# Kernel tuning notes

Measured on AMD Instinct MI355X. Metric: run time of the kernel, lower is better.

Reference implementation:

```python
import math
import jax, jax.numpy as jnp
import numpy as np

B, N, D, H = 2, 8192, 1024, 16


def setup_inputs() -> dict:
    key = jax.random.key(0)
    k1, k2, k3, k4 = jax.random.split(key, 4)
    s = 1.0 / math.sqrt(D)
    return {
        "x": jax.random.normal(k1, (B, N, D), dtype=jnp.float32),
        "W_qk": jax.random.normal(k2, (D, D), dtype=jnp.float32) * s,
        "W_v": jax.random.normal(k3, (D, D), dtype=jnp.float32) * s,
        "W_out": jax.random.normal(k4, (D, D), dtype=jnp.float32) * s,
        "tau": jnp.ones((H, 1, 1), dtype=jnp.float32),
    }


def reference(x, W_qk, W_v, W_out, tau):
    b, n, d = x.shape
    h = H
    dh = d // h
    # QK / V projections (no bias), then to channel-major (B, H, dh, N)
    qk = (x @ W_qk).transpose(0, 2, 1).reshape(b, h, dh, n)
    v = (x @ W_v).transpose(0, 2, 1).reshape(b, h, dh, n)
    # Cross-channel Gram matrix over tokens: (B, H, dh, dh)
    dot = jnp.einsum('bhcn,bhdn->bhcd', qk, qk)
    q2 = jnp.sum(qk * qk, axis=-1)  # (B, H, dh)
    # Negative squared Euclidean distance between channel vectors
    logits = (2.0 * dot - q2[:, :, :, None] - q2[:, :, None, :]) / math.sqrt(max(n, 1))
    logits = logits * tau[None, ...]
    attn = jax.nn.softmax(logits, axis=-1)  # (B, H, dh, dh)
    w = jnp.einsum('bhcd,bhdn->bhcn', attn, v)  # (B, H, dh, N)
    out = w.reshape(b, d, n).transpose(0, 2, 1) @ W_out  # (B, N, D)
    return out
```

## Files before the change

### kernel.cpp

```cpp
#include <hip/hip_runtime.h>
#include <hip/hip_bf16.h>
#include <cstdint>
#include <cstddef>

typedef __bf16 v8bf __attribute__((ext_vector_type(8)));
typedef float  v4f  __attribute__((ext_vector_type(4)));

__device__ __forceinline__ unsigned short f2bf(float f) {
    unsigned int u = __float_as_uint(f);
    u += 0x7fffu + ((u >> 16) & 1u);
    return (unsigned short)(u >> 16);
}

__device__ __forceinline__ void gload_lds16(const unsigned short* g, unsigned short* l) {
    __builtin_amdgcn_global_load_lds(
        (const __attribute__((address_space(1))) unsigned int*)(uintptr_t)g,
        (__attribute__((address_space(3))) unsigned int*)(uintptr_t)l, 16, 0, 0);
}

template<int WRITE_BF16>
__global__ __launch_bounds__(256, 2) void gemm_bt(
    const unsigned short* __restrict__ A,
    const unsigned short* __restrict__ BT,
    void* __restrict__ C,
    int K, int lda, int ldb, int ldc,
    size_t sAz, size_t sBz, size_t sCz,
    int nBlk, int mPerXcd)
{
    __shared__ unsigned short sA[128 * 32];
    __shared__ unsigned short sB[128 * 32];

    const int id = blockIdx.x;
    const int xcd = id & 7;
    int s = id >> 3;
    const int perXcd = mPerXcd * nBlk;
    const int z = s / perXcd;
    s -= z * perXcd;
    const int mB = xcd * mPerXcd + s / nBlk;
    const int nB = s - (s / nBlk) * nBlk;

    const unsigned short* Ab = A + (size_t)z * sAz;
    const unsigned short* Bb = BT + (size_t)z * sBz;

    const int tid  = threadIdx.x;
    const int wv   = tid >> 6;
    const int lane = tid & 63;
    const int quad = lane >> 4;
    const int l16  = lane & 15;
    const size_t bm = (size_t)mB * 128;
    const size_t bn = (size_t)nB * 128;
    const int wm = (wv >> 1) * 64;
    const int wn = (wv & 1) * 64;

    const int ro = tid >> 2;
    const int ko = (((tid & 3) ^ (ro & 3)) << 3);

    const unsigned short* aptr0 = Ab + (bm + ro)      * (size_t)lda + ko;
    const unsigned short* aptr1 = Ab + (bm + ro + 64) * (size_t)lda + ko;
    const unsigned short* bptr0 = Bb + (bn + ro)      * (size_t)ldb + ko;
    const unsigned short* bptr1 = Bb + (bn + ro + 64) * (size_t)ldb + ko;

    unsigned short* sA0 = &sA[wv * 512];
    unsigned short* sA1 = &sA[2048 + wv * 512];
    unsigned short* sB0 = &sB[wv * 512];
    unsigned short* sB1 = &sB[2048 + wv * 512];

    const int sslot = ((quad ^ (l16 & 3)) << 3);

    v4f acc[4][4] = {};

    for (int k0 = 0; k0 < K; k0 += 32) {
        gload_lds16(aptr0 + k0, sA0);
        gload_lds16(aptr1 + k0, sA1);
        gload_lds16(bptr0 + k0, sB0);
        gload_lds16(bptr1 + k0, sB1);
        __syncthreads();

        v8bf af[4], bfr[4];
        #pragma unroll
        for (int t = 0; t < 4; t++) {
            af[t]  = *(const v8bf*)&sA[(size_t)(wm + t * 16 + l16) * 32 + sslot];
            bfr[t] = *(const v8bf*)&sB[(size_t)(wn + t * 16 + l16) * 32 + sslot];
        }

        #pragma unroll
        for (int ti = 0; ti < 4; ti++)
            #pragma unroll
            for (int tj = 0; tj < 4; tj++)
                acc[ti][tj] = __builtin_amdgcn_mfma_f32_16x16x32_bf16(
                    af[ti], bfr[tj], acc[ti][tj], 0, 0, 0);
        __syncthreads();
    }

    if (WRITE_BF16) {
        unsigned short* Cb = (unsigned short*)C + (size_t)z * sCz;
        #pragma unroll
        for (int ti = 0; ti < 4; ti++) {
            const size_t row0 = bm + wm + ti * 16 + quad * 4;
            #pragma unroll
            for (int tj = 0; tj < 4; tj++) {
                const size_t col = bn + wn + tj * 16 + l16;
                #pragma unroll
                for (int r = 0; r < 4; r++)
                    Cb[(row0 + r) * (size_t)ldc + col] = f2bf(acc[ti][tj][r]);
            }
        }
    } else {
        float* Cb = (float*)C + (size_t)z * sCz;
        #pragma unroll
        for (int ti = 0; ti < 4; ti++) {
            const size_t row0 = bm + wm + ti * 16 + quad * 4;
            #pragma unroll
            for (int tj = 0; tj < 4; tj++) {
                const size_t col = bn + wn + tj * 16 + l16;
                #pragma unroll
                for (int r = 0; r < 4; r++)
                    Cb[(row0 + r) * (size_t)ldc + col] = acc[ti][tj][r];
            }
        }
    }
}

#define MFMA_Q(MH, NH, BF)                                                    \
    do {                                                                      \
        __builtin_amdgcn_s_setprio(1);                                        \
        _Pragma("unroll")                                                     \
        for (int mi = 0; mi < 4; ++mi) {                                      \
            _Pragma("unroll")                                                 \
            for (int ni = 0; ni < 2; ++ni) {                                  \
                acc[(MH)*4 + mi][(NH)*2 + ni] =                               \
                    __builtin_amdgcn_mfma_f32_16x16x32_bf16(                  \
                        aF[mi][0], BF[ni][0],                                 \
                        acc[(MH)*4 + mi][(NH)*2 + ni], 0, 0, 0);              \
                acc[(MH)*4 + mi][(NH)*2 + ni] =                               \
                    __builtin_amdgcn_mfma_f32_16x16x32_bf16(                  \
                        aF[mi][1], BF[ni][1],                                 \
                        acc[(MH)*4 + mi][(NH)*2 + ni], 0, 0, 0);              \
            }                                                                 \
        }                                                                     \
        __builtin_amdgcn_s_setprio(0);                                        \
    } while (0)

#define RD_A(BASE)                                                            \
    do {                                                                      \
        _Pragma("unroll")                                                     \
        for (int mi = 0; mi < 4; ++mi) {                                      \
            aF[mi][0] = *(const v8bf*)((BASE) + (arow0 + mi * 1024));         \
            aF[mi][1] = *(const v8bf*)((BASE) + ((arow0 + mi * 1024) ^ 32));  \
        }                                                                     \
    } while (0)

#define RD_B(DST, BASE)                                                       \
    do {                                                                      \
        _Pragma("unroll")                                                     \
        for (int ni = 0; ni < 2; ++ni) {                                      \
            DST[ni][0] = *(const v8bf*)((BASE) + (brow0 + ni * 1024));        \
            DST[ni][1] = *(const v8bf*)((BASE) + ((brow0 + ni * 1024) ^ 32)); \
        }                                                                     \
    } while (0)

#define GTILE(T, P, B0CUR, B0NXT)                                             \
    do {                                                                      \
        const unsigned short* sa = sm + (P) * 16384;                          \
        const unsigned short* sb = sm + 32768 + (P) * 16384;                  \
        unsigned short* dq = sm + ((P) ^ 1) * 16384;                          \
        unsigned short* dp = sm + (P) * 16384;                                \
        const int kk1 = ((T) + 1) * 64, kk2 = ((T) + 2) * 64;                 \
                                                       \
        RD_A(sa);                                                             \
        if ((T) + 1 < NT) {                                                   \
            gload_lds16(aP + 128 * lda + kk1, dq + 8192 + stA);               \
            gload_lds16(aP + 192 * lda + kk1, dq + 8192 + stA + 4096);        \
        }                                                                     \
        __builtin_amdgcn_s_barrier();                                         \
        asm volatile("s_waitcnt lgkmcnt(0)" ::: "memory");                    \
        __builtin_amdgcn_sched_barrier(0);                                    \
        MFMA_Q(0, 0, B0CUR);                                                  \
        __builtin_amdgcn_s_barrier();                                         \
                                                       \
        RD_B(b1, sb + 8192);                                                  \
        if ((T) + 2 < NT) {                                                   \
            gload_lds16(aP + kk2,            dp + stA);                       \
            gload_lds16(aP + 64 * lda + kk2, dp + stA + 4096);                \
        }                                                                     \
        __builtin_amdgcn_s_barrier();                                         \
        asm volatile("s_waitcnt lgkmcnt(0)" ::: "memory");                    \
        __builtin_amdgcn_sched_barrier(0);                                    \
        MFMA_Q(0, 1, b1);                                                     \
        __builtin_amdgcn_s_barrier();                                         \
                                                       \
        RD_A(sa + 8192);                                                      \
        if ((T) + 2 < NT) {                                                   \
            gload_lds16(bP + kk2,            dp + 32768 + stA);               \
            gload_lds16(bP + 64 * ldb + kk2, dp + 32768 + stA + 4096);        \
        }                                                                     \
        __builtin_amdgcn_s_barrier();                                         \
        asm volatile("s_waitcnt lgkmcnt(0)" ::: "memory");                    \
        __builtin_amdgcn_sched_barrier(0);                                    \
        MFMA_Q(1, 1, b1);                                                     \
        __builtin_amdgcn_s_barrier();                                         \
                                                       \
        if ((T) + 2 < NT) {                                                   \
            gload_lds16(bP + 128 * ldb + kk2, dp + 32768 + 8192 + stA);       \
            gload_lds16(bP + 192 * ldb + kk2, dp + 32768 + 8192 + stA + 4096);\
            asm volatile("s_waitcnt vmcnt(6)" ::: "memory");                  \
        } else {                                                              \
            asm volatile("s_waitcnt vmcnt(0)" ::: "memory");                  \
        }                                                                     \
        if ((T) + 1 < NT) {                                                   \
            RD_B(B0NXT, sm + 32768 + ((P) ^ 1) * 16384);                      \
            asm volatile("" ::: "memory");                                    \
        }                                                                     \
        __builtin_amdgcn_s_barrier();                                         \
        MFMA_Q(1, 0, B0CUR);                                                  \
        __builtin_amdgcn_s_barrier();                                         \
    } while (0)

template<int WRITE_BF16>
__global__ __launch_bounds__(512, 2) void gemm256_bt(
    const unsigned short* __restrict__ A,
    const unsigned short* __restrict__ BT,
    void* __restrict__ C,
    int K, int lda, int ldb, int ldc,
    size_t sAz, size_t sBz, size_t sCz,
    int nBlk, int mPerXcd)
{
    __shared__ unsigned short sm[65536];

    const int id = blockIdx.x;
    const int xcd = id & 7;
    int s = id >> 3;
    const int perXcd = mPerXcd * nBlk;
    const int z = s / perXcd;
    s -= z * perXcd;
    const int mB = xcd * mPerXcd + s / nBlk;
    const int nB = s - (s / nBlk) * nBlk;

    const unsigned short* Ab = A + (size_t)z * sAz;
    const unsigned short* Bb = BT + (size_t)z * sBz;

    const int tid  = threadIdx.x;
    const int wv   = tid >> 6;
    const int lane = tid & 63;
    const int quad = lane >> 4;
    const int l16  = lane & 15;
    const int wm   = wv >> 2;
    const int wn   = wv & 3;

    const size_t bm = (size_t)mB * 256;
    const size_t bn = (size_t)nB * 256;

    const int r0   = tid >> 3;
    const int slog = (tid & 7) ^ (r0 & 7);
    const unsigned short* aP = Ab + (bm + r0) * (size_t)lda + slog * 8;
    const unsigned short* bP = Bb + (bn + r0) * (size_t)ldb + slog * 8;

    const int stA = wv * 512;

    const int soff0 = (quad ^ (l16 & 7)) * 8;
    const int arow0 = (wm * 64 + l16) * 64 + soff0;
    const int brow0 = (wn * 32 + l16) * 64 + soff0;

    v4f  acc[8][4] = {};
    v8bf aF[4][2];
    v8bf b1[2][2];
    v8bf b0a[2][2];
    v8bf b0b[2][2];

    const int NT = K >> 6;

    {
        gload_lds16(aP,                sm + stA);
        gload_lds16(aP + 64 * lda,     sm + stA + 4096);
        gload_lds16(aP + 128 * lda,    sm + 8192 + stA);
        gload_lds16(aP + 192 * lda,    sm + 8192 + stA + 4096);
        gload_lds16(bP,                sm + 32768 + stA);
        gload_lds16(bP + 64 * ldb,     sm + 32768 + stA + 4096);
        gload_lds16(bP + 128 * ldb,    sm + 32768 + 8192 + stA);
        gload_lds16(bP + 192 * ldb,    sm + 32768 + 8192 + stA + 4096);
        gload_lds16(aP + 64,                 sm + 16384 + stA);
        gload_lds16(aP + 64 * lda + 64,      sm + 16384 + stA + 4096);
        gload_lds16(bP + 64,                 sm + 32768 + 16384 + stA);
        gload_lds16(bP + 64 * ldb + 64,      sm + 32768 + 16384 + stA + 4096);
        gload_lds16(bP + 128 * ldb + 64,     sm + 32768 + 16384 + 8192 + stA);
        gload_lds16(bP + 192 * ldb + 64,     sm + 32768 + 16384 + 8192 + stA + 4096);
        asm volatile("s_waitcnt vmcnt(6)" ::: "memory");
        __builtin_amdgcn_s_barrier();
        RD_B(b0a, sm + 32768);
        asm volatile("" ::: "memory");
    }

    for (int it = 0; it < (NT >> 1); ++it) {
        const int t0 = it * 2;
        GTILE(t0,     0, b0a, b0b);
        GTILE(t0 + 1, 1, b0b, b0a);
    }

    if (WRITE_BF16) {
        unsigned short* Cb = (unsigned short*)C + (size_t)z * sCz;
        #pragma unroll
        for (int mh = 0; mh < 2; ++mh)
            #pragma unroll
            for (int mi = 0; mi < 4; ++mi) {
                const size_t row0 = bm + mh * 128 + wm * 64 + mi * 16 + quad * 4;
                #pragma unroll
                for (int nh = 0; nh < 2; ++nh)
                    #pragma unroll
                    for (int ni = 0; ni < 2; ++ni) {
                        const size_t col = bn + nh * 128 + wn * 32 + ni * 16 + l16;
                        #pragma unroll
                        for (int r = 0; r < 4; ++r)
                            Cb[(row0 + r) * (size_t)ldc + col] =
                                f2bf(acc[mh * 4 + mi][nh * 2 + ni][r]);
                    }
            }
    } else {
        float* Cb = (float*)C + (size_t)z * sCz;
        #pragma unroll
        for (int mh = 0; mh < 2; ++mh)
            #pragma unroll
            for (int mi = 0; mi < 4; ++mi) {
                const size_t row0 = bm + mh * 128 + wm * 64 + mi * 16 + quad * 4;
                #pragma unroll
                for (int nh = 0; nh < 2; ++nh)
                    #pragma unroll
                    for (int ni = 0; ni < 2; ++ni) {
                        const size_t col = bn + nh * 128 + wn * 32 + ni * 16 + l16;
                        #pragma unroll
                        for (int r = 0; r < 4; ++r)
                            Cb[(row0 + r) * (size_t)ldc + col] =
                                acc[mh * 4 + mi][nh * 2 + ni][r];
                    }
            }
    }
}
#undef GTILE
#undef RD_A
#undef RD_B
#undef MFMA_Q

__global__ __launch_bounds__(256) void gram_kernel(
    const unsigned short* __restrict__ qk,
    float* __restrict__ partial)
{
    const int bh = blockIdx.x;
    const int split = blockIdx.y;
    const int b = bh >> 4, h = bh & 15;
    const unsigned short* base = qk + (size_t)b * 8192 * 1024 + (size_t)h * 64;
    const int n0 = split * 512;

    __shared__ unsigned short sMT[64 * 136];
    const int tid = threadIdx.x;
    const int wv = tid >> 6, lane = tid & 63, quad = lane >> 4, l16 = lane & 15;

    uint4 pre[4];
    #pragma unroll
    for (int i = 0; i < 4; i++) {
        const int ch = tid + i * 256, tok = ch >> 3, co = (ch & 7) << 3;
        pre[i] = *(const uint4*)(base + (size_t)(n0 + tok) * 1024 + co);
    }

    v4f acc[4] = {};

    for (int chunk = 0; chunk < 4; chunk++) {
        __syncthreads();
        #pragma unroll
        for (int i = 0; i < 4; i++) {
            const int ch = tid + i * 256, tok = ch >> 3, co = (ch & 7) << 3;
            union { uint4 v; unsigned short s8[8]; } u; u.v = pre[i];
            #pragma unroll
            for (int j = 0; j < 8; j++)
                sMT[(size_t)(co + j) * 136 + tok] = u.s8[j];
        }
        __syncthreads();

        if (chunk < 3) {
            const int nb = n0 + (chunk + 1) * 128;
            #pragma unroll
            for (int i = 0; i < 4; i++) {
                const int ch = tid + i * 256, tok = ch >> 3, co = (ch & 7) << 3;
                pre[i] = *(const uint4*)(base + (size_t)(nb + tok) * 1024 + co);
            }
        }

        #pragma unroll
        for (int ks = 0; ks < 4; ks++) {
            const int kb = ks * 32 + quad * 8;
            const v8bf a = *(const v8bf*)&sMT[(size_t)(16 * wv + l16) * 136 + kb];
            #pragma unroll
            for (int t = 0; t < 4; t++) {
                const v8bf bb = *(const v8bf*)&sMT[(size_t)(t * 16 + l16) * 136 + kb];
                acc[t] = __builtin_amdgcn_mfma_f32_16x16x32_bf16(a, bb, acc[t], 0, 0, 0);
            }
        }
    }

    float* outp = partial + ((size_t)split * 32 + bh) * 4096;
    #pragma unroll
    for (int t = 0; t < 4; t++)
        #pragma unroll
        for (int r = 0; r < 4; r++)
            outp[(size_t)(16 * wv + quad * 4 + r) * 64 + t * 16 + l16] = acc[t][r];
}

__global__ __launch_bounds__(256) void softmax_kernel(
    const float* __restrict__ partial,
    const float* __restrict__ tau,
    float* __restrict__ attnT)
{
    const int gw = (int)((blockIdx.x * 256 + threadIdx.x) >> 6);
    const int d = threadIdx.x & 63;
    const int bh = gw >> 6;
    const int c = gw & 63;
    const int h = bh & 15;

    float cd = 0.f, cc = 0.f, dd = 0.f;
    #pragma unroll
    for (int s = 0; s < 16; s++) {
        const float* p = partial + ((size_t)s * 32 + bh) * 4096;
        cd += p[c * 64 + d];
        cc += p[c * 65];
        dd += p[d * 65];
    }
    const float INV_SQRT_N = 0.011048543456039806f;
    const float logit = (2.f * cd - cc - dd) * INV_SQRT_N * tau[h];

    float m = logit;
    #pragma unroll
    for (int off = 32; off > 0; off >>= 1) m = fmaxf(m, __shfl_xor(m, off, 64));
    const float e = __expf(logit - m);
    float sum = e;
    #pragma unroll
    for (int off = 32; off > 0; off >>= 1) sum += __shfl_xor(sum, off, 64);

    attnT[(size_t)bh * 4096 + d * 64 + c] = e / sum;
}

__global__ __launch_bounds__(256) void wefft_kernel(
    const float* __restrict__ attnT,
    const float* __restrict__ Wout,
    unsigned short* __restrict__ weffT)
{
    const int bh = blockIdx.x;
    const int jg = blockIdx.y;
    const int b = bh >> 4, h = bh & 15;

    __shared__ float sAttT[64][65];
    __shared__ float sW[64][65];
    const int tid = threadIdx.x;
    const float* ap = attnT + (size_t)bh * 4096;
    const float* wp = Wout + (size_t)(h * 64) * 1024 + jg * 64;
    for (int i = tid; i < 4096; i += 256) {
        const int r = i >> 6, q = i & 63;
        sAttT[r][q] = ap[i];
        sW[r][q] = wp[(size_t)r * 1024 + q];
    }
    __syncthreads();

    const int dd0 = (tid >> 4) << 2;
    const int j0  = (tid & 15) << 2;
    float acc[4][4] = {};
    for (int cc = 0; cc < 64; cc++) {
        float av[4], wvv[4];
        #pragma unroll
        for (int i = 0; i < 4; i++) av[i] = sAttT[dd0 + i][cc];
        #pragma unroll
        for (int i = 0; i < 4; i++) wvv[i] = sW[cc][j0 + i];
        #pragma unroll
        for (int i = 0; i < 4; i++)
            #pragma unroll
            for (int j = 0; j < 4; j++)
                acc[i][j] += av[i] * wvv[j];
    }

    unsigned short* op = weffT + ((size_t)b * 1024 + jg * 64) * 1024 + h * 64;
    #pragma unroll
    for (int i = 0; i < 4; i++)
        #pragma unroll
        for (int j = 0; j < 4; j++)
            op[(size_t)(j0 + j) * 1024 + dd0 + i] = f2bf(acc[i][j]);
}

__global__ __launch_bounds__(256) void cvt_all_kernel(
    const float* __restrict__ x, const float* __restrict__ Wv,
    const float* __restrict__ Wqk,
    unsigned short* __restrict__ xb, unsigned short* __restrict__ wvb,
    unsigned short* __restrict__ wqkT)
{
    const int bid = blockIdx.x;
    if (bid < 17408) {
        const float* src = (bid < 16384) ? x : Wv;
        unsigned short* dst = (bid < 16384) ? xb : wvb;
        const size_t blk = (bid < 16384) ? bid : (bid - 16384);
        const size_t i = (blk * 256 + threadIdx.x) * 4;
        const float4 v = *(const float4*)(src + i);
        ushort4 o;
        o.x = f2bf(v.x); o.y = f2bf(v.y); o.z = f2bf(v.z); o.w = f2bf(v.w);
        *(ushort4*)(dst + i) = o;
    } else {
        const int t = bid - 17408;
        const int n0 = (t & 31) * 32, k0 = (t >> 5) * 32;
        __shared__ float sT[32][33];
        const int tx = threadIdx.x & 31, ty = threadIdx.x >> 5;
        #pragma unroll
        for (int i = ty; i < 32; i += 8)
            sT[i][tx] = Wqk[(size_t)(k0 + i) * 1024 + n0 + tx];
        __syncthreads();
        #pragma unroll
        for (int i = ty; i < 32; i += 8)
            wqkT[(size_t)(n0 + i) * 1024 + k0 + tx] = f2bf(sT[tx][i]);
    }
}

extern "C" void kernel_launch(void* const* d_in, const int* in_sizes, int n_in,
                              void* d_out, int out_size, void* d_ws, size_t ws_size,
                              hipStream_t stream)
{
    (void)in_sizes; (void)n_in; (void)out_size; (void)ws_size;
    const float* x    = (const float*)d_in[0];
    const float* Wqk  = (const float*)d_in[1];
    const float* Wv   = (const float*)d_in[2];
    const float* Wout = (const float*)d_in[3];
    const float* tau  = (const float*)d_in[4];

    unsigned short* xb     = (unsigned short*)d_ws;
    unsigned short* wqkT   = xb + (size_t)16384 * 1024;
    unsigned short* wvb    = wqkT + (size_t)1024 * 1024;
    unsigned short* qk     = wvb + (size_t)1024 * 1024;
    float*          partial= (float*)(qk + (size_t)16384 * 1024);
    float*          attnT  = partial + (size_t)16 * 32 * 4096;
    unsigned short* weffT  = (unsigned short*)(attnT + (size_t)32 * 4096);
    unsigned short* wfoldT = weffT + (size_t)2 * 1024 * 1024;

    cvt_all_kernel<<<18432, 256, 0, stream>>>(x, Wv, Wqk, xb, wvb, wqkT);

    gemm256_bt<1><<<256, 512, 0, stream>>>(
        xb, wqkT, (void*)qk, 1024, 1024, 1024, 1024, 0, 0, 0, 4, 8);

    gram_kernel<<<dim3(32, 16), 256, 0, stream>>>(qk, partial);
    softmax_kernel<<<512, 256, 0, stream>>>(partial, tau, attnT);
    wefft_kernel<<<dim3(32, 16), 256, 0, stream>>>(attnT, Wout, weffT);

    gemm_bt<1><<<128, 256, 0, stream>>>(
        weffT, wvb, (void*)wfoldT, 1024, 1024, 1024, 1024,
        (size_t)1024 * 1024, 0, (size_t)1024 * 1024, 8, 1);

    gemm256_bt<0><<<256, 512, 0, stream>>>(
        xb, wfoldT, d_out, 1024, 1024, 1024, 1024,
        (size_t)8192 * 1024, (size_t)1024 * 1024, (size_t)8192 * 1024, 4, 4);
}
```

Measured before the change: 264.4 us.

## Produce QK projection channel-major so gram kernel reads it without transposing

The QK projection GEMM now swaps its operands (W_qk^T times x^T), so it writes qk in channel-major layout (1024 x 16384). A new swapBig flag keeps the XCD-aware block mapping on the large dimension. The gram kernel then loads whole 64x512 channel slices straight into a swizzled LDS buffer with async global-to-LDS copies, replacing the per-element transpose through shared memory. The GEMM macro helpers are inlined and the sched_barriers removed, which leaves the compiler freer to reorder instructions but loosens the hand-tuned schedule.

```diff
diff --git a/kernel.cpp b/kernel.cpp
--- a/kernel.cpp
+++ b/kernel.cpp
@@ -141,24 +141,6 @@
         __builtin_amdgcn_s_setprio(0);                                        \
     } while (0)
 
-#define RD_A(BASE)                                                            \
-    do {                                                                      \
-        _Pragma("unroll")                                                     \
-        for (int mi = 0; mi < 4; ++mi) {                                      \
-            aF[mi][0] = *(const v8bf*)((BASE) + (arow0 + mi * 1024));         \
-            aF[mi][1] = *(const v8bf*)((BASE) + ((arow0 + mi * 1024) ^ 32));  \
-        }                                                                     \
-    } while (0)
-
-#define RD_B(DST, BASE)                                                       \
-    do {                                                                      \
-        _Pragma("unroll")                                                     \
-        for (int ni = 0; ni < 2; ++ni) {                                      \
-            DST[ni][0] = *(const v8bf*)((BASE) + (brow0 + ni * 1024));        \
-            DST[ni][1] = *(const v8bf*)((BASE) + ((brow0 + ni * 1024) ^ 32)); \
-        }                                                                     \
-    } while (0)
-
 #define GTILE(T, P, B0CUR, B0NXT)                                             \
     do {                                                                      \
         const unsigned short* sa = sm + (P) * 16384;                          \
@@ -166,40 +148,49 @@
         unsigned short* dq = sm + ((P) ^ 1) * 16384;                          \
         unsigned short* dp = sm + (P) * 16384;                                \
         const int kk1 = ((T) + 1) * 64, kk2 = ((T) + 2) * 64;                 \
-                                                       \
-        RD_A(sa);                                                             \
+                             \
+        _Pragma("unroll")                                                     \
+        for (int mi = 0; mi < 4; ++mi) {                                      \
+            aF[mi][0] = *(const v8bf*)(sa + (arow0 + mi * 1024));             \
+            aF[mi][1] = *(const v8bf*)(sa + ((arow0 + mi * 1024) ^ 32));      \
+        }                                                                     \
         if ((T) + 1 < NT) {                                                   \
             gload_lds16(aP + 128 * lda + kk1, dq + 8192 + stA);               \
             gload_lds16(aP + 192 * lda + kk1, dq + 8192 + stA + 4096);        \
         }                                                                     \
         __builtin_amdgcn_s_barrier();                                         \
         asm volatile("s_waitcnt lgkmcnt(0)" ::: "memory");                    \
-        __builtin_amdgcn_sched_barrier(0);                                    \
         MFMA_Q(0, 0, B0CUR);                                                  \
         __builtin_amdgcn_s_barrier();                                         \
-                                                       \
-        RD_B(b1, sb + 8192);                                                  \
+                             \
+        _Pragma("unroll")                                                     \
+        for (int ni = 0; ni < 2; ++ni) {                                      \
+            b1[ni][0] = *(const v8bf*)(sb + 8192 + (brow0 + ni * 1024));      \
+            b1[ni][1] = *(const v8bf*)(sb + 8192 + ((brow0 + ni * 1024) ^ 32));\
+        }                                                                     \
         if ((T) + 2 < NT) {                                                   \
             gload_lds16(aP + kk2,            dp + stA);                       \
             gload_lds16(aP + 64 * lda + kk2, dp + stA + 4096);                \
         }                                                                     \
         __builtin_amdgcn_s_barrier();                                         \
         asm volatile("s_waitcnt lgkmcnt(0)" ::: "memory");                    \
-        __builtin_amdgcn_sched_barrier(0);                                    \
         MFMA_Q(0, 1, b1);                                                     \
         __builtin_amdgcn_s_barrier();                                         \
-                                                       \
-        RD_A(sa + 8192);                                                      \
+                             \
+        _Pragma("unroll")                                                     \
+        for (int mi = 0; mi < 4; ++mi) {                                      \
+            aF[mi][0] = *(const v8bf*)(sa + 8192 + (arow0 + mi * 1024));      \
+            aF[mi][1] = *(const v8bf*)(sa + 8192 + ((arow0 + mi * 1024) ^ 32));\
+        }                                                                     \
         if ((T) + 2 < NT) {                                                   \
             gload_lds16(bP + kk2,            dp + 32768 + stA);               \
             gload_lds16(bP + 64 * ldb + kk2, dp + 32768 + stA + 4096);        \
         }                                                                     \
         __builtin_amdgcn_s_barrier();                                         \
         asm volatile("s_waitcnt lgkmcnt(0)" ::: "memory");                    \
-        __builtin_amdgcn_sched_barrier(0);                                    \
         MFMA_Q(1, 1, b1);                                                     \
         __builtin_amdgcn_s_barrier();                                         \
-                                                       \
+            \
         if ((T) + 2 < NT) {                                                   \
             gload_lds16(bP + 128 * ldb + kk2, dp + 32768 + 8192 + stA);       \
             gload_lds16(bP + 192 * ldb + kk2, dp + 32768 + 8192 + stA + 4096);\
@@ -208,7 +199,12 @@
             asm volatile("s_waitcnt vmcnt(0)" ::: "memory");                  \
         }                                                                     \
         if ((T) + 1 < NT) {                                                   \
-            RD_B(B0NXT, sm + 32768 + ((P) ^ 1) * 16384);                      \
+            const unsigned short* nb = sm + 32768 + ((P) ^ 1) * 16384;        \
+            _Pragma("unroll")                                                 \
+            for (int ni = 0; ni < 2; ++ni) {                                  \
+                B0NXT[ni][0] = *(const v8bf*)(nb + (brow0 + ni * 1024));      \
+                B0NXT[ni][1] = *(const v8bf*)(nb + ((brow0 + ni * 1024) ^ 32));\
+            }                                                                 \
             asm volatile("" ::: "memory");                                    \
         }                                                                     \
         __builtin_amdgcn_s_barrier();                                         \
@@ -223,7 +219,7 @@
     void* __restrict__ C,
     int K, int lda, int ldb, int ldc,
     size_t sAz, size_t sBz, size_t sCz,
-    int nBlk, int mPerXcd)
+    int nBlk, int mPerXcd, int swapBig)
 {
     __shared__ unsigned short sm[65536];
 
@@ -233,8 +229,10 @@
     const int perXcd = mPerXcd * nBlk;
     const int z = s / perXcd;
     s -= z * perXcd;
-    const int mB = xcd * mPerXcd + s / nBlk;
-    const int nB = s - (s / nBlk) * nBlk;
+    const int bigB   = xcd * mPerXcd + s / nBlk;
+    const int smallB = s - (s / nBlk) * nBlk;
+    const int mB = swapBig ? smallB : bigB;
+    const int nB = swapBig ? bigB : smallB;
 
     const unsigned short* Ab = A + (size_t)z * sAz;
     const unsigned short* Bb = BT + (size_t)z * sBz;
@@ -286,7 +284,11 @@
         gload_lds16(bP + 192 * ldb + 64,     sm + 32768 + 16384 + 8192 + stA + 4096);
         asm volatile("s_waitcnt vmcnt(6)" ::: "memory");
         __builtin_amdgcn_s_barrier();
-        RD_B(b0a, sm + 32768);
+        #pragma unroll
+        for (int ni = 0; ni < 2; ++ni) {
+            b0a[ni][0] = *(const v8bf*)(sm + 32768 + (brow0 + ni * 1024));
+            b0a[ni][1] = *(const v8bf*)(sm + 32768 + ((brow0 + ni * 1024) ^ 32));
+        }
         asm volatile("" ::: "memory");
     }
 
@@ -335,63 +337,43 @@
     }
 }
 #undef GTILE
-#undef RD_A
-#undef RD_B
 #undef MFMA_Q
 
-__global__ __launch_bounds__(256) void gram_kernel(
-    const unsigned short* __restrict__ qk,
+__global__ __launch_bounds__(256, 2) void gram_kernel(
+    const unsigned short* __restrict__ qkT,
     float* __restrict__ partial)
 {
     const int bh = blockIdx.x;
     const int split = blockIdx.y;
     const int b = bh >> 4, h = bh & 15;
-    const unsigned short* base = qk + (size_t)b * 8192 * 1024 + (size_t)h * 64;
-    const int n0 = split * 512;
-
-    __shared__ unsigned short sMT[64 * 136];
+    const unsigned short* base =
+        qkT + (size_t)(h * 64) * 16384 + (size_t)b * 8192 + (size_t)split * 512;
+
+    __shared__ unsigned short sM[64 * 512];
     const int tid = threadIdx.x;
     const int wv = tid >> 6, lane = tid & 63, quad = lane >> 4, l16 = lane & 15;
 
-    uint4 pre[4];
-    #pragma unroll
-    for (int i = 0; i < 4; i++) {
-        const int ch = tid + i * 256, tok = ch >> 3, co = (ch & 7) << 3;
-        pre[i] = *(const uint4*)(base + (size_t)(n0 + tok) * 1024 + co);
-    }
+    #pragma unroll
+    for (int i = 0; i < 16; i++) {
+        const int row = i * 4 + wv;
+        const int lo  = (lane & 56) | ((lane & 7) ^ (row & 7));
+        gload_lds16(base + (size_t)row * 16384 + lo * 8,
+                    sM + (size_t)i * 2048 + wv * 512);
+    }
+    __syncthreads();
 
     v4f acc[4] = {};
-
-    for (int chunk = 0; chunk < 4; chunk++) {
-        __syncthreads();
-        #pragma unroll
-        for (int i = 0; i < 4; i++) {
-            const int ch = tid + i * 256, tok = ch >> 3, co = (ch & 7) << 3;
-            union { uint4 v; unsigned short s8[8]; } u; u.v = pre[i];
-            #pragma unroll
-            for (int j = 0; j < 8; j++)
-                sMT[(size_t)(co + j) * 136 + tok] = u.s8[j];
-        }
-        __syncthreads();
-
-        if (chunk < 3) {
-            const int nb = n0 + (chunk + 1) * 128;
-            #pragma unroll
-            for (int i = 0; i < 4; i++) {
-                const int ch = tid + i * 256, tok = ch >> 3, co = (ch & 7) << 3;
-                pre[i] = *(const uint4*)(base + (size_t)(nb + tok) * 1024 + co);
-            }
-        }
-
-        #pragma unroll
-        for (int ks = 0; ks < 4; ks++) {
-            const int kb = ks * 32 + quad * 8;
-            const v8bf a = *(const v8bf*)&sMT[(size_t)(16 * wv + l16) * 136 + kb];
-            #pragma unroll
-            for (int t = 0; t < 4; t++) {
-                const v8bf bb = *(const v8bf*)&sMT[(size_t)(t * 16 + l16) * 136 + kb];
-                acc[t] = __builtin_amdgcn_mfma_f32_16x16x32_bf16(a, bb, acc[t], 0, 0, 0);
-            }
+    const int cha = 16 * wv + l16;
+
+    #pragma unroll
+    for (int ks = 0; ks < 16; ks++) {
+        const int lg = ks * 4 + quad;
+        const int so = ((lg & 56) | ((lg & 7) ^ (l16 & 7))) * 8;
+        const v8bf a = *(const v8bf*)&sM[(size_t)cha * 512 + so];
+        #pragma unroll
+        for (int t = 0; t < 4; t++) {
+            const v8bf bb = *(const v8bf*)&sM[(size_t)(t * 16 + l16) * 512 + so];
+            acc[t] = __builtin_amdgcn_mfma_f32_16x16x32_bf16(a, bb, acc[t], 0, 0, 0);
         }
     }
 
@@ -526,8 +508,8 @@
     unsigned short* xb     = (unsigned short*)d_ws;
     unsigned short* wqkT   = xb + (size_t)16384 * 1024;
     unsigned short* wvb    = wqkT + (size_t)1024 * 1024;
-    unsigned short* qk     = wvb + (size_t)1024 * 1024;
-    float*          partial= (float*)(qk + (size_t)16384 * 1024);
+    unsigned short* qkT    = wvb + (size_t)1024 * 1024;
+    float*          partial= (float*)(qkT + (size_t)16384 * 1024);
     float*          attnT  = partial + (size_t)16 * 32 * 4096;
     unsigned short* weffT  = (unsigned short*)(attnT + (size_t)32 * 4096);
     unsigned short* wfoldT = weffT + (size_t)2 * 1024 * 1024;
@@ -535,9 +517,9 @@
     cvt_all_kernel<<<18432, 256, 0, stream>>>(x, Wv, Wqk, xb, wvb, wqkT);
 
     gemm256_bt<1><<<256, 512, 0, stream>>>(
-        xb, wqkT, (void*)qk, 1024, 1024, 1024, 1024, 0, 0, 0, 4, 8);
-
-    gram_kernel<<<dim3(32, 16), 256, 0, stream>>>(qk, partial);
+        wqkT, xb, (void*)qkT, 1024, 1024, 1024, 16384, 0, 0, 0, 4, 8, 1);
+
+    gram_kernel<<<dim3(32, 16), 256, 0, stream>>>(qkT, partial);
     softmax_kernel<<<512, 256, 0, stream>>>(partial, tau, attnT);
     wefft_kernel<<<dim3(32, 16), 256, 0, stream>>>(attnT, Wout, weffT);
 
@@ -547,5 +529,5 @@
 
     gemm256_bt<0><<<256, 512, 0, stream>>>(
         xb, wfoldT, d_out, 1024, 1024, 1024, 1024,
-        (size_t)8192 * 1024, (size_t)1024 * 1024, (size_t)8192 * 1024, 4, 4);
-}
+        (size_t)8192 * 1024, (size_t)1024 * 1024, (size_t)8192 * 1024, 4, 4, 0);
+}
```

Result: no change. 262.3 us (-0.8%).
